# Optimization experiments

Hardware: AMD Instinct MI355X
Metric: run time of the kernel (lower is better)

## Reference

```python
import jax, jax.numpy as jnp
import numpy as np


def setup_inputs() -> dict:
    key = jax.random.key(0)
    k1, k2, k3 = jax.random.split(key, 3)
    B, NF, Fm, H, NC = 4, 4096, 32, 128, 256
    x = jax.random.normal(k1, (B, NF, Fm, H), dtype=jnp.float32)
    segment_ids = jax.random.randint(k2, (NF,), 0, NC)  # fine -> coarse assignment
    W = jax.random.normal(k3, (1, H), dtype=jnp.float32) / np.sqrt(H)  # Linear(H, 1) weight
    b = jnp.zeros((1,), dtype=jnp.float32)                              # Linear(H, 1) bias
    return {"x": x, "W": W, "b": b, "segment_ids": segment_ids, "num_coarse": NC}


def reference(x, W, b, segment_ids, num_coarse):
    # x: [B, NF, Fm, H]; scores = Linear(mean over Fm) -> [B, NF]
    scores = jnp.einsum('bnh,h->bn', x.mean(axis=2), W[0]) + b[0]

    def per_batch(s, xi):
        # segmented stable softmax over fine nodes within each coarse group
        smax = jax.ops.segment_max(s, segment_ids, num_segments=num_coarse)
        e = jnp.exp(s - smax[segment_ids])
        denom = jax.ops.segment_sum(e, segment_ids, num_segments=num_coarse)
        w = e / denom[segment_ids]                      # [NF]
        # score-weighted scatter-reduce into coarse nodes: [NC, Fm, H]
        return jax.ops.segment_sum(w[:, None, None] * xi, segment_ids,
                                   num_segments=num_coarse)

    return jax.vmap(per_batch)(scores, x)  # [B, NC, Fm, H]
```

## Files before the change

kernel.cpp:

```cpp
#include <hip/hip_runtime.h>
#include <math.h>

#define B   4
#define NF  4096
#define FM  32
#define H   128
#define NC  256
#define ROW (FM * H)
#define RQ  (ROW / 4)

__global__ __launch_bounds__(256) void k_fused(const float* __restrict__ x,
                                               const float* __restrict__ W,
                                               const float* __restrict__ bias,
                                               const int* __restrict__ seg,
                                               float* __restrict__ out) {
    __shared__ __align__(16) int cnt[NC];
    __shared__ int   scn[256];
    __shared__ int   list[NF];
    __shared__ float red[8];
    __shared__ int   s_c[2];
    __shared__ int   s_m;

    const int t    = threadIdx.x;
    const int wid  = t >> 6;
    const int lane = t & 63;
    const int pr   = blockIdx.x >> 2;
    const int b    = blockIdx.x & 3;

    int sv[16];
    cnt[t] = 0;
    __syncthreads();
    {
        const int4* s4 = (const int4*)seg;
#pragma unroll
        for (int k = 0; k < 4; ++k) {
            int4 v = s4[t * 4 + k];
            sv[k * 4 + 0] = v.x; sv[k * 4 + 1] = v.y;
            sv[k * 4 + 2] = v.z; sv[k * 4 + 3] = v.w;
        }
#pragma unroll
        for (int k = 0; k < 16; ++k)
            atomicAdd(&cnt[sv[k]], 1);
    }
    __syncthreads();

    {
        const int my = cnt[t];
        int r = 0;
        const int4* c4 = (const int4*)cnt;
#pragma unroll
        for (int j = 0; j < 64; ++j) {
            const int4 cv = c4[j];
            const int base = j * 4;
            r += (cv.x > my) || (cv.x == my && (base + 0) < t);
            r += (cv.y > my) || (cv.y == my && (base + 1) < t);
            r += (cv.z > my) || (cv.z == my && (base + 2) < t);
            r += (cv.w > my) || (cv.w == my && (base + 3) < t);
        }
        if (r == pr)       s_c[0] = t;
        if (r == 255 - pr) s_c[1] = t;
    }
    __syncthreads();

    const float4 w4     = ((const float4*)W)[t & 31];
    const float  inv_fm = 1.0f / FM;
    const float  b0     = bias[0];
    const float4* xb    = (const float4*)x + (size_t)b * NF * RQ;

    for (int half = 0; half < 2; ++half) {
        const int c = s_c[half];

        int loc = 0;
#pragma unroll
        for (int k = 0; k < 16; ++k) loc += (sv[k] == c);
        scn[t] = loc;
        __syncthreads();
        for (int d = 1; d < 256; d <<= 1) {
            int v = (t >= d) ? scn[t - d] : 0;
            __syncthreads();
            scn[t] += v;
            __syncthreads();
        }
        if (t == 255) s_m = scn[255];
        int pos = scn[t] - loc;
        __syncthreads();
#pragma unroll
        for (int k = 0; k < 16; ++k)
            if (sv[k] == c) list[pos++] = t * 16 + k;
        __syncthreads();
        const int m = s_m;

        float4 acc0 = {0,0,0,0}, acc1 = {0,0,0,0};
        float4 acc2 = {0,0,0,0}, acc3 = {0,0,0,0};
        float  mx = -INFINITY, denom = 0.f;

        float4 c0, c1, c2, c3;
        if (m > 0) {
            const float4* rp = xb + (size_t)list[0] * RQ + t;
            c0 = rp[0]; c1 = rp[256]; c2 = rp[512]; c3 = rp[768];
        }

        for (int r = 0; r < m; ++r) {
            float4 n0, n1, n2, n3;
            const bool more = (r + 1 < m);
            if (more) {
                const float4* np = xb + (size_t)list[r + 1] * RQ + t;
                n0 = np[0]; n1 = np[256]; n2 = np[512]; n3 = np[768];
            }

            float p = (c0.x + c1.x + c2.x + c3.x) * w4.x
                    + (c0.y + c1.y + c2.y + c3.y) * w4.y
                    + (c0.z + c1.z + c2.z + c3.z) * w4.z
                    + (c0.w + c1.w + c2.w + c3.w) * w4.w;
#pragma unroll
            for (int off = 32; off >= 1; off >>= 1)
                p += __shfl_xor(p, off, 64);
            if (lane == 0) red[(r & 1) * 4 + wid] = p;
            __syncthreads();
            const int sl = (r & 1) * 4;
            const float s = (red[sl] + red[sl+1] + red[sl+2] + red[sl+3])
                            * inv_fm + b0;

            if (s > mx) {
                const float scale = __expf(mx - s);
                denom *= scale;
                acc0.x *= scale; acc0.y *= scale; acc0.z *= scale; acc0.w *= scale;
                acc1.x *= scale; acc1.y *= scale; acc1.z *= scale; acc1.w *= scale;
                acc2.x *= scale; acc2.y *= scale; acc2.z *= scale; acc2.w *= scale;
                acc3.x *= scale; acc3.y *= scale; acc3.z *= scale; acc3.w *= scale;
                mx = s;
            }
            const float e = __expf(s - mx);
            denom += e;
            acc0.x += e * c0.x; acc0.y += e * c0.y; acc0.z += e * c0.z; acc0.w += e * c0.w;
            acc1.x += e * c1.x; acc1.y += e * c1.y; acc1.z += e * c1.z; acc1.w += e * c1.w;
            acc2.x += e * c2.x; acc2.y += e * c2.y; acc2.z += e * c2.z; acc2.w += e * c2.w;
            acc3.x += e * c3.x; acc3.y += e * c3.y; acc3.z += e * c3.z; acc3.w += e * c3.w;

            if (more) { c0 = n0; c1 = n1; c2 = n2; c3 = n3; }
        }

        const float inv = (denom > 0.f) ? (1.0f / denom) : 0.f;
        float4* op = (float4*)(out + (size_t)(b * NC + c) * ROW) + t;
        acc0.x *= inv; acc0.y *= inv; acc0.z *= inv; acc0.w *= inv;
        acc1.x *= inv; acc1.y *= inv; acc1.z *= inv; acc1.w *= inv;
        acc2.x *= inv; acc2.y *= inv; acc2.z *= inv; acc2.w *= inv;
        acc3.x *= inv; acc3.y *= inv; acc3.z *= inv; acc3.w *= inv;
        op[0] = acc0; op[256] = acc1; op[512] = acc2; op[768] = acc3;

        __syncthreads();
    }
}

extern "C" void kernel_launch(void* const* d_in, const int* in_sizes, int n_in,
                              void* d_out, int out_size, void* d_ws, size_t ws_size,
                              hipStream_t stream) {
    const float* x    = (const float*)d_in[0];
    const float* W    = (const float*)d_in[1];
    const float* bias = (const float*)d_in[2];
    const int*   seg  = (const int*)d_in[3];
    float*       out  = (float*)d_out;

    k_fused<<<(NC / 2) * B, 256, 0, stream>>>(x, W, bias, seg, out);
}
```

Before: 57.93 us.

## Use 512-thread blocks, process two rows per iteration, build lists with atomics

Each block now runs 512 threads, so each thread holds two float4s of a row instead of four. Every loop iteration handles two fine rows, which halves the number of block-wide barriers per row, and it prefetches the next two rows so more loads are in flight. The per-group prefix scan is replaced with a shared-memory atomic counter, and the group size now comes from the histogram. In exchange, the order of rows in the list is no longer deterministic, so floating-point summation order varies from run to run. The larger block may also limit how many blocks fit on each compute unit.

```diff
diff --git a/kernel.cpp b/kernel.cpp
--- a/kernel.cpp
+++ b/kernel.cpp
@@ -8,18 +8,20 @@
 #define NC  256
 #define ROW (FM * H)
 #define RQ  (ROW / 4)
+#define NT  512
+#define SPT (NF / NT)
 
-__global__ __launch_bounds__(256) void k_fused(const float* __restrict__ x,
-                                               const float* __restrict__ W,
-                                               const float* __restrict__ bias,
-                                               const int* __restrict__ seg,
-                                               float* __restrict__ out) {
+__global__ __launch_bounds__(NT, 4) void k_fused(const float* __restrict__ x,
+                                                 const float* __restrict__ W,
+                                                 const float* __restrict__ bias,
+                                                 const int* __restrict__ seg,
+                                                 float* __restrict__ out) {
     __shared__ __align__(16) int cnt[NC];
-    __shared__ int   scn[256];
     __shared__ int   list[NF];
-    __shared__ float red[8];
+    __shared__ float redA[16];
+    __shared__ float redB[16];
     __shared__ int   s_c[2];
-    __shared__ int   s_m;
+    __shared__ int   s_cur;
 
     const int t    = threadIdx.x;
     const int wid  = t >> 6;
@@ -27,28 +29,28 @@
     const int pr   = blockIdx.x >> 2;
     const int b    = blockIdx.x & 3;
 
-    int sv[16];
-    cnt[t] = 0;
+    int sv[SPT];
+    if (t < NC) cnt[t] = 0;
     __syncthreads();
     {
         const int4* s4 = (const int4*)seg;
 #pragma unroll
-        for (int k = 0; k < 4; ++k) {
-            int4 v = s4[t * 4 + k];
+        for (int k = 0; k < SPT / 4; ++k) {
+            int4 v = s4[t * (SPT / 4) + k];
             sv[k * 4 + 0] = v.x; sv[k * 4 + 1] = v.y;
             sv[k * 4 + 2] = v.z; sv[k * 4 + 3] = v.w;
         }
 #pragma unroll
-        for (int k = 0; k < 16; ++k)
+        for (int k = 0; k < SPT; ++k)
             atomicAdd(&cnt[sv[k]], 1);
     }
     __syncthreads();
 
-    {
+    if (t < NC) {
         const int my = cnt[t];
         int r = 0;
         const int4* c4 = (const int4*)cnt;
-#pragma unroll
+#pragma unroll 16
         for (int j = 0; j < 64; ++j) {
             const int4 cv = c4[j];
             const int base = j * 4;
@@ -69,84 +71,78 @@
 
     for (int half = 0; half < 2; ++half) {
         const int c = s_c[half];
+        const int m = cnt[c];
 
-        int loc = 0;
-#pragma unroll
-        for (int k = 0; k < 16; ++k) loc += (sv[k] == c);
-        scn[t] = loc;
-        __syncthreads();
-        for (int d = 1; d < 256; d <<= 1) {
-            int v = (t >= d) ? scn[t - d] : 0;
-            __syncthreads();
-            scn[t] += v;
-            __syncthreads();
-        }
-        if (t == 255) s_m = scn[255];
-        int pos = scn[t] - loc;
+        if (t == 0) s_cur = 0;
         __syncthreads();
 #pragma unroll
-        for (int k = 0; k < 16; ++k)
-            if (sv[k] == c) list[pos++] = t * 16 + k;
+        for (int k = 0; k < SPT; ++k)
+            if (sv[k] == c) list[atomicAdd(&s_cur, 1)] = t * SPT + k;
         __syncthreads();
-        const int m = s_m;
 
-        float4 acc0 = {0,0,0,0}, acc1 = {0,0,0,0};
-        float4 acc2 = {0,0,0,0}, acc3 = {0,0,0,0};
+        float4 a0 = {0,0,0,0}, a1 = {0,0,0,0};
         float  mx = -INFINITY, denom = 0.f;
 
-        float4 c0, c1, c2, c3;
-        if (m > 0) {
-            const float4* rp = xb + (size_t)list[0] * RQ + t;
-            c0 = rp[0]; c1 = rp[256]; c2 = rp[512]; c3 = rp[768];
-        }
+        float4 c0 = {0,0,0,0}, c1 = {0,0,0,0};
+        float4 d0 = {0,0,0,0}, d1 = {0,0,0,0};
+        if (m > 0) { const float4* p = xb + (size_t)list[0] * RQ + t; c0 = p[0]; c1 = p[NT]; }
+        if (m > 1) { const float4* p = xb + (size_t)list[1] * RQ + t; d0 = p[0]; d1 = p[NT]; }
 
-        for (int r = 0; r < m; ++r) {
+        int par = 0;
+        for (int r = 0; r < m; r += 2, par ^= 1) {
             float4 n0, n1, n2, n3;
-            const bool more = (r + 1 < m);
-            if (more) {
-                const float4* np = xb + (size_t)list[r + 1] * RQ + t;
-                n0 = np[0]; n1 = np[256]; n2 = np[512]; n3 = np[768];
+            const bool h2 = (r + 1 < m);
+            const bool h3 = (r + 2 < m);
+            const bool h4 = (r + 3 < m);
+            if (h3) { const float4* p = xb + (size_t)list[r + 2] * RQ + t; n0 = p[0]; n1 = p[NT]; }
+            if (h4) { const float4* p = xb + (size_t)list[r + 3] * RQ + t; n2 = p[0]; n3 = p[NT]; }
+
+            float p0 = (c0.x + c1.x) * w4.x + (c0.y + c1.y) * w4.y
+                     + (c0.z + c1.z) * w4.z + (c0.w + c1.w) * w4.w;
+            float p1 = (d0.x + d1.x) * w4.x + (d0.y + d1.y) * w4.y
+                     + (d0.z + d1.z) * w4.z + (d0.w + d1.w) * w4.w;
+#pragma unroll
+            for (int off = 32; off >= 1; off >>= 1) {
+                p0 += __shfl_xor(p0, off, 64);
+                p1 += __shfl_xor(p1, off, 64);
             }
+            if (lane == 0) { redA[par * 8 + wid] = p0; redB[par * 8 + wid] = p1; }
+            __syncthreads();
+            float s0 = 0.f, s1 = 0.f;
+#pragma unroll
+            for (int i = 0; i < 8; ++i) {
+                s0 += redA[par * 8 + i];
+                s1 += redB[par * 8 + i];
+            }
+            s0 = s0 * inv_fm + b0;
+            s1 = h2 ? (s1 * inv_fm + b0) : -INFINITY;
 
-            float p = (c0.x + c1.x + c2.x + c3.x) * w4.x
-                    + (c0.y + c1.y + c2.y + c3.y) * w4.y
-                    + (c0.z + c1.z + c2.z + c3.z) * w4.z
-                    + (c0.w + c1.w + c2.w + c3.w) * w4.w;
-#pragma unroll
-            for (int off = 32; off >= 1; off >>= 1)
-                p += __shfl_xor(p, off, 64);
-            if (lane == 0) red[(r & 1) * 4 + wid] = p;
-            __syncthreads();
-            const int sl = (r & 1) * 4;
-            const float s = (red[sl] + red[sl+1] + red[sl+2] + red[sl+3])
-                            * inv_fm + b0;
+            const float m2 = fmaxf(s0, s1);
+            if (m2 > mx) {
+                const float sc = __expf(mx - m2);
+                denom *= sc;
+                a0.x *= sc; a0.y *= sc; a0.z *= sc; a0.w *= sc;
+                a1.x *= sc; a1.y *= sc; a1.z *= sc; a1.w *= sc;
+                mx = m2;
+            }
+            const float e0 = __expf(s0 - mx);
+            const float e1 = h2 ? __expf(s1 - mx) : 0.f;
+            denom += e0 + e1;
+            a0.x += e0 * c0.x + e1 * d0.x; a0.y += e0 * c0.y + e1 * d0.y;
+            a0.z += e0 * c0.z + e1 * d0.z; a0.w += e0 * c0.w + e1 * d0.w;
+            a1.x += e0 * c1.x + e1 * d1.x; a1.y += e0 * c1.y + e1 * d1.y;
+            a1.z += e0 * c1.z + e1 * d1.z; a1.w += e0 * c1.w + e1 * d1.w;
 
-            if (s > mx) {
-                const float scale = __expf(mx - s);
-                denom *= scale;
-                acc0.x *= scale; acc0.y *= scale; acc0.z *= scale; acc0.w *= scale;
-                acc1.x *= scale; acc1.y *= scale; acc1.z *= scale; acc1.w *= scale;
-                acc2.x *= scale; acc2.y *= scale; acc2.z *= scale; acc2.w *= scale;
-                acc3.x *= scale; acc3.y *= scale; acc3.z *= scale; acc3.w *= scale;
-                mx = s;
-            }
-            const float e = __expf(s - mx);
-            denom += e;
-            acc0.x += e * c0.x; acc0.y += e * c0.y; acc0.z += e * c0.z; acc0.w += e * c0.w;
-            acc1.x += e * c1.x; acc1.y += e * c1.y; acc1.z += e * c1.z; acc1.w += e * c1.w;
-            acc2.x += e * c2.x; acc2.y += e * c2.y; acc2.z += e * c2.z; acc2.w += e * c2.w;
-            acc3.x += e * c3.x; acc3.y += e * c3.y; acc3.z += e * c3.z; acc3.w += e * c3.w;
-
-            if (more) { c0 = n0; c1 = n1; c2 = n2; c3 = n3; }
+            if (h3) { c0 = n0; c1 = n1; }
+            if (h4) { d0 = n2; d1 = n3; }
         }
 
         const float inv = (denom > 0.f) ? (1.0f / denom) : 0.f;
         float4* op = (float4*)(out + (size_t)(b * NC + c) * ROW) + t;
-        acc0.x *= inv; acc0.y *= inv; acc0.z *= inv; acc0.w *= inv;
-        acc1.x *= inv; acc1.y *= inv; acc1.z *= inv; acc1.w *= inv;
-        acc2.x *= inv; acc2.y *= inv; acc2.z *= inv; acc2.w *= inv;
-        acc3.x *= inv; acc3.y *= inv; acc3.z *= inv; acc3.w *= inv;
-        op[0] = acc0; op[256] = acc1; op[512] = acc2; op[768] = acc3;
+        a0.x *= inv; a0.y *= inv; a0.z *= inv; a0.w *= inv;
+        a1.x *= inv; a1.y *= inv; a1.z *= inv; a1.w *= inv;
+        op[0]  = a0;
+        op[NT] = a1;
 
         __syncthreads();
     }
@@ -161,5 +157,5 @@
     const int*   seg  = (const int*)d_in[3];
     float*       out  = (float*)d_out;
 
-    k_fused<<<(NC / 2) * B, 256, 0, stream>>>(x, W, bias, seg, out);
+    k_fused<<<(NC / 2) * B, NT, 0, stream>>>(x, W, bias, seg, out);
 }
```

Result: faster. 54.51 us (-5.9%).
